# Kernel tuning notes

Hardware: AMD Instinct MI355X
Metric: run time of the kernel (lower is better)

## Reference

```python
import jax, jax.numpy as jnp
import numpy as np

B = 4096


def setup_inputs() -> dict:
    key = jax.random.key(0)
    u = jax.random.uniform(key, (B, 5), dtype=jnp.float32)
    centers = u[:, :2] * 64.0          # box centers in [0, 64)
    wh = u[:, 2:4] * 8.0 + 1.0         # widths/heights in [1, 9)
    ang = u[:, 4:5] * 3.14159265       # rotation angle in [0, pi)
    boxes = jnp.concatenate([centers, wh, ang], axis=-1)  # (B,5)
    return {"boxes": boxes}


def _rect_to_corners(boxes):
    # boxes: (B,5) = (x, y, w, h, theta) -> corners (B,4,2)
    unit = jnp.array([[-1.0, -1.0], [1.0, -1.0], [1.0, 1.0], [-1.0, 1.0]],
                     dtype=boxes.dtype)
    ctr, wh, ang = boxes[:, :2], boxes[:, 2:4], boxes[:, 4]
    base = unit[None, :, :] * (wh * 0.5)[:, None, :]        # (B,4,2)
    c, s = jnp.cos(ang), jnp.sin(ang)
    rot = jnp.stack([jnp.stack([c, -s], -1),
                     jnp.stack([s, c], -1)], axis=1)         # (B,2,2)
    return jnp.einsum('bkd,bde->bke', base, rot) + ctr[:, None, :]


def _giou1d(min1, max1, min2, max2):
    # exact (non-fast) 1-D GIoU per axis
    inter = jnp.clip(jnp.minimum(max1, max2) - jnp.maximum(min1, min2), 0.0)
    union = (max1 - min1) + (max2 - min2) - inter
    hull = jnp.maximum(max1, max2) - jnp.minimum(min1, min2)
    return inter / union - (hull - union) / hull


def reference(boxes):
    corners = _rect_to_corners(boxes)                        # (B,4,2)
    nb = corners.shape[0]
    # two edge axes per box: c1-c0 and c3-c0
    axes = jnp.stack([corners[:, 1] - corners[:, 0],
                      corners[:, 3] - corners[:, 0]], axis=1)  # (B,2,2)
    # self projections: box b's corners onto its own axes
    sp = jnp.einsum('bkd,bad->bak', corners, axes)           # (B,2,4)
    smin, smax = sp.min(-1), sp.max(-1)                      # (B,2)
    # cross projections: corners of box i onto axes of box j
    cp = jnp.einsum('ikd,jad->ijak', corners, axes)          # (B,B,2,4)
    cmin, cmax = cp.min(-1), cp.max(-1)                      # (B,B,2)
    # projections of box j's corners onto box i's axes = transpose of cross
    cminT, cmaxT = jnp.swapaxes(cmin, 0, 1), jnp.swapaxes(cmax, 0, 1)
    # axes of box i: (box i self) vs (box j projected on i's axes)
    gA = _giou1d(smin[:, None, :], smax[:, None, :], cminT, cmaxT)  # (B,B,2)
    # axes of box j: (box i projected on j's axes) vs (box j self)
    gB = _giou1d(cmin, cmax, smin[None, :, :], smax[None, :, :])    # (B,B,2)
    g = jnp.concatenate([gA, gB], axis=-1).min(-1)           # min over 4 axes
    pairwise = jnp.clip(g, 0.0)
    idx = jnp.arange(nb)
    pairwise = pairwise.at[idx, idx].set(0.0)                # zero diagonal
    return pairwise  # reduction='none' -> (B,B)
```

## Files before the change

kernel.cpp:

```cpp
#include <hip/hip_runtime.h>
#include <math.h>

#define NBOX 4096
#define TILE 64
#define NT (NBOX / TILE)
#define NBLK (NT * (NT + 1) / 2)
#define SS 12
#define JBASE (TILE * SS)

typedef float vfloat4 __attribute__((ext_vector_type(4)));


struct Box {
    float cx, cy, a0x, a0y, a1x, a1y, sc0, sc1, l0, l1;
};

__device__ __forceinline__ float rcp_fast(float x) {
    return __builtin_amdgcn_rcpf(x);
}

__device__ __forceinline__ float giou_axis1(float H1, float H2, float D) {
    float S = H1 + H2;
    float u = fmaf(0.5f, S, -fabsf(D));
    float r = fminf(fminf(H1, H2), u);
    return r * rcp_fast(S - r);
}

__device__ __forceinline__ float mgiou_pair(const Box& I, const Box& J) {
    float d00 = fmaf(I.a0x, J.a0x, I.a0y * J.a0y);
    float d01 = fmaf(I.a0x, J.a1x, I.a0y * J.a1y);
    float d10 = fmaf(I.a1x, J.a0x, I.a1y * J.a0y);
    float d11 = fmaf(I.a1x, J.a1x, I.a1y * J.a1y);
    float DI0 = fmaf(I.a0x, J.cx, fmaf(I.a0y, J.cy, -I.sc0));
    float DI1 = fmaf(I.a1x, J.cx, fmaf(I.a1y, J.cy, -I.sc1));
    float DJ0 = fmaf(J.a0x, I.cx, fmaf(J.a0y, I.cy, -J.sc0));
    float DJ1 = fmaf(J.a1x, I.cx, fmaf(J.a1y, I.cy, -J.sc1));
    float HI0 = fabsf(d00) + fabsf(d01);
    float HI1 = fabsf(d10) + fabsf(d11);
    float HJ0 = fabsf(d00) + fabsf(d10);
    float HJ1 = fabsf(d01) + fabsf(d11);
    float g0 = giou_axis1(I.l0, HI0, DI0);
    float g1 = giou_axis1(I.l1, HI1, DI1);
    float g2 = giou_axis1(J.l0, HJ0, DJ0);
    float g3 = giou_axis1(J.l1, HJ1, DJ1);
    float g = fminf(fminf(g0, g1), fminf(g2, g3));
    return fmaxf(g, 0.0f);
}

__device__ __forceinline__ int j_offset(int j) {
    return JBASE + j * SS + (j >> 3) * 4;
}

__device__ __forceinline__ Box load_box(const float* p) {
    Box b;
    float4 x = *(const float4*)(p);
    float4 y = *(const float4*)(p + 4);
    float2 z = *(const float2*)(p + 8);
    b.cx = x.x;  b.cy = x.y;  b.a0x = x.z; b.a0y = x.w;
    b.a1x = y.x; b.a1y = y.y; b.sc0 = y.z; b.sc1 = y.w;
    b.l0 = z.x;  b.l1 = z.y;
    return b;
}

__global__ __launch_bounds__(256)
void pairwise_kernel(const float* __restrict__ boxes, float* __restrict__ out) {
    int k = blockIdx.x;
    int bi = (int)((float)(2 * NT + 1 - sqrtf((float)((2 * NT + 1) * (2 * NT + 1) - 8 * k))) * 0.5f);
    if (bi > 0 && k < bi * NT - bi * (bi - 1) / 2) bi--;
    if (k >= (bi + 1) * NT - (bi + 1) * bi / 2) bi++;
    int bj = bi + (k - (bi * NT - bi * (bi - 1) / 2));

    __shared__ float sm[JBASE + TILE * SS + ((TILE - 1) >> 3) * 4 + 8];
    __shared__ float tileT[TILE][TILE + 1];

    int tid = threadIdx.x;
    if (tid < 2 * TILE) {
        int loc = tid & (TILE - 1);
        int box = ((tid < TILE) ? bi : bj) * TILE + loc;
        float cx = boxes[box * 5 + 0];
        float cy = boxes[box * 5 + 1];
        float w  = boxes[box * 5 + 2];
        float h  = boxes[box * 5 + 3];
        float ang = boxes[box * 5 + 4];
        float s, c;
        __sincosf(ang, &s, &c);
        float a0x = w * c, a0y = -w * s;
        float a1x = h * s, a1y =  h * c;
        float sc0 = fmaf(a0x, cx, a0y * cy);
        float sc1 = fmaf(a1x, cx, a1y * cy);
        float* d = &sm[(tid < TILE) ? (loc * SS) : j_offset(loc)];
        ((float4*)d)[0] = make_float4(cx, cy, a0x, a0y);
        ((float4*)d)[1] = make_float4(a1x, a1y, sc0, sc1);
        ((float2*)d)[4] = make_float2(w * w, h * h);
    }
    __syncthreads();

    int tx = tid & 15;
    int ty = tid >> 4;
    Box I[4], J[4];
    #pragma unroll
    for (int kk = 0; kk < 4; ++kk) I[kk] = load_box(&sm[(ty + 16 * kk) * SS]);
    const float* jp = &sm[j_offset(4 * tx)];
    #pragma unroll
    for (int m = 0; m < 4; ++m) J[m] = load_box(jp + m * SS);

    int ibase = bi * TILE, jbase = bj * TILE;
    float v[4][4];
    #pragma unroll
    for (int kk = 0; kk < 4; ++kk) {
        int ig = ibase + ty + 16 * kk;
        #pragma unroll
        for (int m = 0; m < 4; ++m) {
            int jg = jbase + 4 * tx + m;
            v[kk][m] = (ig == jg) ? 0.0f : mgiou_pair(I[kk], J[m]);
        }
    }

    #pragma unroll
    for (int kk = 0; kk < 4; ++kk) {
        int ig = ibase + ty + 16 * kk;
        vfloat4 o = {v[kk][0], v[kk][1], v[kk][2], v[kk][3]};
        __builtin_nontemporal_store(o, (vfloat4*)&out[(size_t)ig * NBOX + jbase + 4 * tx]);
    }

    #pragma unroll
    for (int kk = 0; kk < 4; ++kk)
        #pragma unroll
        for (int m = 0; m < 4; ++m)
            tileT[ty + 16 * kk][4 * tx + m] = v[kk][m];
    __syncthreads();

    #pragma unroll
    for (int kk = 0; kk < 4; ++kk) {
        int jl = ty + 16 * kk;
        vfloat4 o = {tileT[4 * tx + 0][jl], tileT[4 * tx + 1][jl],
                     tileT[4 * tx + 2][jl], tileT[4 * tx + 3][jl]};
        __builtin_nontemporal_store(o, (vfloat4*)&out[(size_t)(jbase + jl) * NBOX + ibase + 4 * tx]);
    }
}

extern "C" void kernel_launch(void* const* d_in, const int* in_sizes, int n_in,
                              void* d_out, int out_size, void* d_ws, size_t ws_size,
                              hipStream_t stream) {
    const float* boxes = (const float*)d_in[0];
    float* out = (float*)d_out;
    pairwise_kernel<<<dim3(NBLK), dim3(256), 0, stream>>>(boxes, out);
}
```

Measured before the change: 81.99 us.

## Use 4x4 register micro-tiles with direct transposed stores and packed float2 math

Result: no change. 82.36 us (+0.5%).

```diff
diff --git a/kernel.cpp b/kernel.cpp
--- a/kernel.cpp
+++ b/kernel.cpp
@@ -6,59 +6,58 @@
 #define NT (NBOX / TILE)
 #define NBLK (NT * (NT + 1) / 2)
 #define SS 12
-#define JBASE (TILE * SS)
+#define JB 800
 
-typedef float vfloat4 __attribute__((ext_vector_type(4)));
+typedef float v2f __attribute__((ext_vector_type(2)));
+typedef float vf4 __attribute__((ext_vector_type(4)));
 
 
 struct Box {
-    float cx, cy, a0x, a0y, a1x, a1y, sc0, sc1, l0, l1;
+    v2f A0, A1, SC, LL;
+    float cx, cy;
 };
 
-__device__ __forceinline__ float rcp_fast(float x) {
-    return __builtin_amdgcn_rcpf(x);
-}
-
-__device__ __forceinline__ float giou_axis1(float H1, float H2, float D) {
-    float S = H1 + H2;
-    float u = fmaf(0.5f, S, -fabsf(D));
-    float r = fminf(fminf(H1, H2), u);
-    return r * rcp_fast(S - r);
-}
+__device__ __forceinline__ float rcp_fast(float x) { return __builtin_amdgcn_rcpf(x); }
+__device__ __forceinline__ v2f splat(float s) { return (v2f){s, s}; }
+__device__ __forceinline__ v2f fma2(v2f a, v2f b, v2f c) { return __builtin_elementwise_fma(a, b, c); }
+__device__ __forceinline__ v2f abs2(v2f a) { return __builtin_elementwise_abs(a); }
 
 __device__ __forceinline__ float mgiou_pair(const Box& I, const Box& J) {
-    float d00 = fmaf(I.a0x, J.a0x, I.a0y * J.a0y);
-    float d01 = fmaf(I.a0x, J.a1x, I.a0y * J.a1y);
-    float d10 = fmaf(I.a1x, J.a0x, I.a1y * J.a0y);
-    float d11 = fmaf(I.a1x, J.a1x, I.a1y * J.a1y);
-    float DI0 = fmaf(I.a0x, J.cx, fmaf(I.a0y, J.cy, -I.sc0));
-    float DI1 = fmaf(I.a1x, J.cx, fmaf(I.a1y, J.cy, -I.sc1));
-    float DJ0 = fmaf(J.a0x, I.cx, fmaf(J.a0y, I.cy, -J.sc0));
-    float DJ1 = fmaf(J.a1x, I.cx, fmaf(J.a1y, I.cy, -J.sc1));
-    float HI0 = fabsf(d00) + fabsf(d01);
-    float HI1 = fabsf(d10) + fabsf(d11);
-    float HJ0 = fabsf(d00) + fabsf(d10);
-    float HJ1 = fabsf(d01) + fabsf(d11);
-    float g0 = giou_axis1(I.l0, HI0, DI0);
-    float g1 = giou_axis1(I.l1, HI1, DI1);
-    float g2 = giou_axis1(J.l0, HJ0, DJ0);
-    float g3 = giou_axis1(J.l1, HJ1, DJ1);
+    v2f dA = fma2(I.A0, splat(J.A0.x), I.A1 * J.A1.x);
+    v2f dB = fma2(I.A0, splat(J.A0.y), I.A1 * J.A1.y);
+    v2f DI = fma2(I.A0, splat(J.cx), fma2(I.A1, splat(J.cy), -I.SC));
+    v2f DJ = fma2(J.A0, splat(I.cx), fma2(J.A1, splat(I.cy), -J.SC));
+    v2f aA = abs2(dA), aB = abs2(dB);
+    v2f HI = aA + aB;
+    float HJ0 = aA.x + aA.y;
+    float HJ1 = aB.x + aB.y;
+    v2f SI = I.LL + HI;
+    float SJ0 = J.LL.x + HJ0, SJ1 = J.LL.y + HJ1;
+    v2f uI = fma2(splat(0.5f), SI, -abs2(DI));
+    float uJ0 = fmaf(0.5f, SJ0, -fabsf(DJ.x));
+    float uJ1 = fmaf(0.5f, SJ1, -fabsf(DJ.y));
+    float r0 = fminf(fminf(I.LL.x, HI.x), uI.x);
+    float r1 = fminf(fminf(I.LL.y, HI.y), uI.y);
+    float r2 = fminf(fminf(J.LL.x, HJ0), uJ0);
+    float r3 = fminf(fminf(J.LL.y, HJ1), uJ1);
+    float g0 = r0 * rcp_fast(SI.x - r0);
+    float g1 = r1 * rcp_fast(SI.y - r1);
+    float g2 = r2 * rcp_fast(SJ0 - r2);
+    float g3 = r3 * rcp_fast(SJ1 - r3);
     float g = fminf(fminf(g0, g1), fminf(g2, g3));
     return fmaxf(g, 0.0f);
 }
 
-__device__ __forceinline__ int j_offset(int j) {
-    return JBASE + j * SS + (j >> 3) * 4;
-}
+__device__ __forceinline__ int sw_offset(int i) { return i * SS + (i >> 3) * 4; }
 
 __device__ __forceinline__ Box load_box(const float* p) {
     Box b;
     float4 x = *(const float4*)(p);
     float4 y = *(const float4*)(p + 4);
     float2 z = *(const float2*)(p + 8);
-    b.cx = x.x;  b.cy = x.y;  b.a0x = x.z; b.a0y = x.w;
-    b.a1x = y.x; b.a1y = y.y; b.sc0 = y.z; b.sc1 = y.w;
-    b.l0 = z.x;  b.l1 = z.y;
+    b.A0 = (v2f){x.x, x.y}; b.A1 = (v2f){x.z, x.w};
+    b.SC = (v2f){y.x, y.y}; b.LL = (v2f){y.z, y.w};
+    b.cx = z.x; b.cy = z.y;
     return b;
 }
 
@@ -70,8 +69,7 @@
     if (k >= (bi + 1) * NT - (bi + 1) * bi / 2) bi++;
     int bj = bi + (k - (bi * NT - bi * (bi - 1) / 2));
 
-    __shared__ float sm[JBASE + TILE * SS + ((TILE - 1) >> 3) * 4 + 8];
-    __shared__ float tileT[TILE][TILE + 1];
+    __shared__ float sm[JB + TILE * SS + ((TILE - 1) >> 3) * 4 + 8];
 
     int tid = threadIdx.x;
     if (tid < 2 * TILE) {
@@ -88,54 +86,47 @@
         float a1x = h * s, a1y =  h * c;
         float sc0 = fmaf(a0x, cx, a0y * cy);
         float sc1 = fmaf(a1x, cx, a1y * cy);
-        float* d = &sm[(tid < TILE) ? (loc * SS) : j_offset(loc)];
-        ((float4*)d)[0] = make_float4(cx, cy, a0x, a0y);
-        ((float4*)d)[1] = make_float4(a1x, a1y, sc0, sc1);
-        ((float2*)d)[4] = make_float2(w * w, h * h);
+        float* d = &sm[((tid < TILE) ? 0 : JB) + sw_offset(loc)];
+        ((float4*)d)[0] = make_float4(a0x, a1x, a0y, a1y);
+        ((float4*)d)[1] = make_float4(sc0, sc1, w * w, h * h);
+        ((float2*)d)[4] = make_float2(cx, cy);
     }
     __syncthreads();
 
     int tx = tid & 15;
     int ty = tid >> 4;
-    Box I[4], J[4];
-    #pragma unroll
-    for (int kk = 0; kk < 4; ++kk) I[kk] = load_box(&sm[(ty + 16 * kk) * SS]);
-    const float* jp = &sm[j_offset(4 * tx)];
+    Box J[4];
+    const float* jp = &sm[JB + sw_offset(4 * tx)];
     #pragma unroll
     for (int m = 0; m < 4; ++m) J[m] = load_box(jp + m * SS);
 
     int ibase = bi * TILE, jbase = bj * TILE;
-    float v[4][4];
+    bool offdiag = (bi != bj);
+    const float* ip = &sm[sw_offset(4 * ty)];
+    float vT[4][4];
+
     #pragma unroll
     for (int kk = 0; kk < 4; ++kk) {
-        int ig = ibase + ty + 16 * kk;
+        Box I = load_box(ip + kk * SS);
+        int ig = ibase + 4 * ty + kk;
+        float v[4];
         #pragma unroll
         for (int m = 0; m < 4; ++m) {
             int jg = jbase + 4 * tx + m;
-            v[kk][m] = (ig == jg) ? 0.0f : mgiou_pair(I[kk], J[m]);
+            v[m] = (ig == jg) ? 0.0f : mgiou_pair(I, J[m]);
+            vT[m][kk] = v[m];
         }
+        vf4 o = {v[0], v[1], v[2], v[3]};
+        __builtin_nontemporal_store(o, (vf4*)&out[(size_t)ig * NBOX + jbase + 4 * tx]);
     }
 
-    #pragma unroll
-    for (int kk = 0; kk < 4; ++kk) {
-        int ig = ibase + ty + 16 * kk;
-        vfloat4 o = {v[kk][0], v[kk][1], v[kk][2], v[kk][3]};
-        __builtin_nontemporal_store(o, (vfloat4*)&out[(size_t)ig * NBOX + jbase + 4 * tx]);
-    }
-
-    #pragma unroll
-    for (int kk = 0; kk < 4; ++kk)
+    if (offdiag) {
         #pragma unroll
-        for (int m = 0; m < 4; ++m)
-            tileT[ty + 16 * kk][4 * tx + m] = v[kk][m];
-    __syncthreads();
-
-    #pragma unroll
-    for (int kk = 0; kk < 4; ++kk) {
-        int jl = ty + 16 * kk;
-        vfloat4 o = {tileT[4 * tx + 0][jl], tileT[4 * tx + 1][jl],
-                     tileT[4 * tx + 2][jl], tileT[4 * tx + 3][jl]};
-        __builtin_nontemporal_store(o, (vfloat4*)&out[(size_t)(jbase + jl) * NBOX + ibase + 4 * tx]);
+        for (int m = 0; m < 4; ++m) {
+            int jg = jbase + 4 * tx + m;
+            vf4 o = {vT[m][0], vT[m][1], vT[m][2], vT[m][3]};
+            __builtin_nontemporal_store(o, (vf4*)&out[(size_t)jg * NBOX + ibase + 4 * ty]);
+        }
     }
 }
 
```
